# Kernel tuning notes

Measured on AMD Instinct MI355X. Metric: run time of the kernel, lower is better.

## Reference

```python
import jax, jax.numpy as jnp
import numpy as np

D = 1024
H = 16
DK = D // H


def setup_inputs() -> dict:
    key = jax.random.key(0)
    ks = jax.random.split(key, 5)
    B, S = 4, 2048
    scale = 1.0 / np.sqrt(D)
    return {
        "inputs": jax.random.normal(ks[0], (B, S, D), dtype=jnp.float32),
        "mask": jnp.ones((B, S), dtype=jnp.int32),
        "Wq": jax.random.normal(ks[1], (D, D), dtype=jnp.float32) * scale,
        "Wk": jax.random.normal(ks[2], (D, D), dtype=jnp.float32) * scale,
        "Wv": jax.random.normal(ks[3], (D, D), dtype=jnp.float32) * scale,
        "Wo": jax.random.normal(ks[4], (D, D), dtype=jnp.float32) * scale,
    }


def reference(inputs, mask, Wq, Wk, Wv, Wo):
    B, S, _ = inputs.shape

    def split_heads(x):  # [B,S,D] -> [B,H,S,DK]
        return x.reshape(B, S, H, DK).transpose(0, 2, 1, 3)

    q = split_heads(inputs @ Wq)
    k = split_heads(inputs @ Wk)
    v = split_heads(inputs @ Wv)

    scores = jnp.einsum("bhqd,bhkd->bhqk", q, k) / jnp.sqrt(jnp.float32(DK))
    m = mask.astype(jnp.float32)[:, None, None, :]  # [B,1,1,S] over key axis
    scores = scores + (1.0 - m) * -1e9
    attn = jax.nn.softmax(scores, axis=-1)
    out = jnp.einsum("bhqk,bhkd->bhqd", attn, v)
    out = out.transpose(0, 2, 1, 3).reshape(B, S, D)
    return out @ Wo
```

## Files before the change

### kernel.cpp

```cpp
#include <hip/hip_runtime.h>
#include <hip/hip_bf16.h>
#include <stdint.h>

#define S_LEN 2048
#define D_DIM 1024
#define NH    16
#define DKH   64
#define BATCH 4

typedef __bf16 bf16x8 __attribute__((ext_vector_type(8)));
typedef float  f32x4  __attribute__((ext_vector_type(4)));

__device__ __forceinline__ unsigned short f2bf(float x) {
  unsigned u = __float_as_uint(x);
  return (unsigned short)((u + 0x7FFFu + ((u >> 16) & 1u)) >> 16);
}
__device__ __forceinline__ float bf2f(unsigned short b) {
  return __uint_as_float(((unsigned)b) << 16);
}

__device__ __forceinline__ void gll16(const void* g, void* l) {
  __builtin_amdgcn_global_load_lds((const __attribute__((address_space(1))) unsigned*)g,
                                   (__attribute__((address_space(3))) unsigned*)l, 16, 0, 0);
}

#define MFMA(a, b, c) __builtin_amdgcn_mfma_f32_16x16x32_bf16(a, b, c, 0, 0, 0)

__global__ void k_split(const float4* __restrict__ x, ushort4* __restrict__ hi,
                        ushort4* __restrict__ lo, int n4) {
  int i = blockIdx.x * 256 + threadIdx.x;
  if (i >= n4) return;
  float4 v = x[i];
  ushort4 h, l;
  h.x = f2bf(v.x); l.x = f2bf(v.x - bf2f(h.x));
  h.y = f2bf(v.y); l.y = f2bf(v.y - bf2f(h.y));
  h.z = f2bf(v.z); l.z = f2bf(v.z - bf2f(h.z));
  h.w = f2bf(v.w); l.w = f2bf(v.w - bf2f(h.w));
  hi[i] = h;
  lo[i] = l;
}

__global__ void k_wt(const float* __restrict__ W, unsigned short* __restrict__ hi,
                     unsigned short* __restrict__ lo) {
  __shared__ float t[64][65];
  const int tid = threadIdx.x;
  const int k0 = blockIdx.x * 64, n0 = blockIdx.y * 64;
#pragma unroll
  for (int i = 0; i < 16; i++) {
    int idx = i * 256 + tid;
    int r = idx >> 6, c = idx & 63;
    t[r][c] = W[(size_t)(k0 + r) * D_DIM + n0 + c];
  }
  __syncthreads();
#pragma unroll
  for (int i = 0; i < 16; i++) {
    int idx = i * 256 + tid;
    int r = idx >> 6, c = idx & 63;
    float v = t[c][r];
    unsigned short h = f2bf(v);
    size_t o = (size_t)(n0 + r) * D_DIM + k0 + c;
    hi[o] = h;
    lo[o] = f2bf(v - bf2f(h));
  }
}

template <int MODE>
__global__ __launch_bounds__(256, 2) void gemm_hilo(
    const unsigned short* __restrict__ Ahi, const unsigned short* __restrict__ Alo,
    const unsigned short* __restrict__ Bth, const unsigned short* __restrict__ Btl,
    unsigned short* __restrict__ Chi, unsigned short* __restrict__ Clo,
    float* __restrict__ Cf, float escale) {
  constexpr int N = 1024, K = 1024;
  extern __shared__ char smem[];
  char* sAh = smem;
  char* sAl = smem + 16384;
  char* sBh = smem + 32768;
  char* sBl = smem + 49152;

  const int tid = threadIdx.x;
  const int lane = tid & 63, w = tid >> 6;
  const int wr = w >> 1, wc = w & 1;
  const int m0 = blockIdx.y * 128, n0 = blockIdx.x * 128;

  int gofs[4], lofs[4];
#pragma unroll
  for (int i = 0; i < 4; i++) {
    int c = (w * 4 + i) * 64 + lane;
    int row = c >> 3, s = c & 7;
    int sp = s ^ (row & 7);
    gofs[i] = row * K + sp * 8;
    lofs[i] = (w * 4 + i) * 1024;
  }
  const unsigned short* pAh = Ahi + (size_t)m0 * K;
  const unsigned short* pAl = Alo + (size_t)m0 * K;
  const unsigned short* pBh = Bth + (size_t)n0 * K;
  const unsigned short* pBl = Btl + (size_t)n0 * K;

  f32x4 acc[4][4] = {};

  for (int kt = 0; kt < K / 64; ++kt) {
    const int ko = kt * 64;
#pragma unroll
    for (int i = 0; i < 4; i++) {
      gll16(pAh + ko + gofs[i], sAh + lofs[i]);
      gll16(pAl + ko + gofs[i], sAl + lofs[i]);
      gll16(pBh + ko + gofs[i], sBh + lofs[i]);
      gll16(pBl + ko + gofs[i], sBl + lofs[i]);
    }
    __syncthreads();
#pragma unroll
    for (int kk = 0; kk < 2; kk++) {
      bf16x8 ah[4], al[4], bh[4], bl[4];
      const int cch = kk * 4 + (lane >> 4);
#pragma unroll
      for (int mr = 0; mr < 4; mr++) {
        int row = wr * 64 + mr * 16 + (lane & 15);
        int off = row * 128 + ((cch ^ (row & 7)) << 4);
        ah[mr] = *(const bf16x8*)(sAh + off);
        al[mr] = *(const bf16x8*)(sAl + off);
      }
#pragma unroll
      for (int nr = 0; nr < 4; nr++) {
        int row = wc * 64 + nr * 16 + (lane & 15);
        int off = row * 128 + ((cch ^ (row & 7)) << 4);
        bh[nr] = *(const bf16x8*)(sBh + off);
        bl[nr] = *(const bf16x8*)(sBl + off);
      }
#pragma unroll
      for (int mr = 0; mr < 4; mr++)
#pragma unroll
        for (int nr = 0; nr < 4; nr++) {
          acc[mr][nr] = MFMA(ah[mr], bh[nr], acc[mr][nr]);
          acc[mr][nr] = MFMA(ah[mr], bl[nr], acc[mr][nr]);
          acc[mr][nr] = MFMA(al[mr], bh[nr], acc[mr][nr]);
        }
    }
    __syncthreads();
  }

#pragma unroll
  for (int mr = 0; mr < 4; mr++)
#pragma unroll
    for (int nr = 0; nr < 4; nr++)
#pragma unroll
      for (int j = 0; j < 4; j++) {
        int row = m0 + wr * 64 + mr * 16 + (lane >> 4) * 4 + j;
        int col = n0 + wc * 64 + nr * 16 + (lane & 15);
        float v = acc[mr][nr][j];
        if constexpr (MODE == 0) {
          v *= escale;
          size_t o = (size_t)row * N + col;
          unsigned short h = f2bf(v);
          Chi[o] = h;
          Clo[o] = f2bf(v - bf2f(h));
        } else if constexpr (MODE == 1) {
          int bi = row >> 11, s = row & (S_LEN - 1);
          int hh = col >> 6, d = col & (DKH - 1);
          size_t o = ((size_t)(bi * NH + hh) * DKH + d) * S_LEN + s;
          unsigned short h = f2bf(v);
          Chi[o] = h;
          Clo[o] = f2bf(v - bf2f(h));
        } else {
          Cf[(size_t)row * N + col] = v;
        }
      }
}

__global__ __launch_bounds__(256, 2) void attn4(
    const unsigned short* __restrict__ Qh, const unsigned short* __restrict__ Ql,
    const unsigned short* __restrict__ Kh, const unsigned short* __restrict__ Kl,
    const unsigned short* __restrict__ Vth, const unsigned short* __restrict__ Vtl,
    const int* __restrict__ mask,
    unsigned short* __restrict__ Oh, unsigned short* __restrict__ Ol) {
  __shared__ char sKh0[8192], sKl0[8192], sVh0[8192], sVl0[8192];
  __shared__ char sKh1[8192], sKl1[8192], sVh1[8192], sVl1[8192];
  __shared__ char sP[4][4096];

  const int tid = threadIdx.x, lane = tid & 63, w = tid >> 6;
  const int bh = blockIdx.x, b = bh >> 4, h = bh & (NH - 1);
  const int q0 = blockIdx.y * 128 + w * 32;
  const int lo16 = lane & 15, hi4 = lane >> 4;

  bf16x8 qh[2][2], ql[2][2];
#pragma unroll
  for (int g = 0; g < 2; g++)
#pragma unroll
    for (int kk = 0; kk < 2; kk++) {
      size_t base = ((size_t)(b * S_LEN + q0 + g * 16 + lo16)) * D_DIM + h * DKH + kk * 32 + hi4 * 8;
      qh[g][kk] = *(const bf16x8*)(Qh + base);
      ql[g][kk] = *(const bf16x8*)(Ql + base);
    }

  int srowK[2], scolK[2], lofs[2];
#pragma unroll
  for (int i = 0; i < 2; i++) {
    int c = (w * 2 + i) * 64 + lane;
    int row = c >> 3, s = c & 7;
    srowK[i] = row;
    scolK[i] = (s ^ (row & 7)) * 8;
    lofs[i] = c * 16 - lane * 16;
  }

  float lsum[2][4] = {};
  f32x4 oacc[2][4] = {};
  char* sPw = sP[w];

  const size_t kbase = (size_t)b * S_LEN * D_DIM + h * DKH;
  const size_t vbase = (size_t)bh * DKH * S_LEN;
  const int* mrow = mask + b * S_LEN;

  auto STAGE = [&](char* dKh, char* dKl, char* dVh, char* dVl, int sk0) {
#pragma unroll
    for (int i = 0; i < 2; i++) {
      size_t gk = kbase + (size_t)(sk0 + srowK[i]) * D_DIM + scolK[i];
      gll16(Kh + gk, dKh + lofs[i]);
      gll16(Kl + gk, dKl + lofs[i]);
      size_t gv = vbase + (size_t)srowK[i] * S_LEN + sk0 + scolK[i];
      gll16(Vth + gv, dVh + lofs[i]);
      gll16(Vtl + gv, dVl + lofs[i]);
    }
  };

  auto COMPUTE = [&](const char* cKh, const char* cKl, const char* cVh,
                     const char* cVl, int sk0) {
    f32x4 sc[2][4] = {};
    __builtin_amdgcn_s_setprio(1);
#pragma unroll
    for (int nr = 0; nr < 4; nr++) {
      int row = nr * 16 + lo16;
      int off0 = row * 128 + ((hi4 ^ (row & 7)) << 4);
      int off1 = row * 128 + (((4 + hi4) ^ (row & 7)) << 4);
      bf16x8 kh0 = *(const bf16x8*)(cKh + off0);
      bf16x8 kh1 = *(const bf16x8*)(cKh + off1);
      bf16x8 kl0 = *(const bf16x8*)(cKl + off0);
      bf16x8 kl1 = *(const bf16x8*)(cKl + off1);
#pragma unroll
      for (int g = 0; g < 2; g++) {
        sc[g][nr] = MFMA(qh[g][0], kh0, sc[g][nr]);
        sc[g][nr] = MFMA(qh[g][1], kh1, sc[g][nr]);
        sc[g][nr] = MFMA(qh[g][0], kl0, sc[g][nr]);
        sc[g][nr] = MFMA(qh[g][1], kl1, sc[g][nr]);
        sc[g][nr] = MFMA(ql[g][0], kh0, sc[g][nr]);
        sc[g][nr] = MFMA(ql[g][1], kh1, sc[g][nr]);
      }
    }
    __builtin_amdgcn_s_setprio(0);

#pragma unroll
    for (int nr = 0; nr < 4; nr++) {
      float bias = mrow[sk0 + nr * 16 + lo16] ? 0.f : -1e9f;
#pragma unroll
      for (int g = 0; g < 2; g++)
#pragma unroll
        for (int j = 0; j < 4; j++) {
          float p = __expf(sc[g][nr][j] + bias);
          lsum[g][j] += p;
          int row = g * 16 + hi4 * 4 + j;
          int colb = (nr * 16 + lo16) * 2;
          *(unsigned short*)(sPw + row * 128 + (colb ^ ((row & 7) << 4))) = f2bf(p);
        }
    }

    bf16x8 pa[2][2];
#pragma unroll
    for (int g = 0; g < 2; g++)
#pragma unroll
      for (int kk = 0; kk < 2; kk++) {
        int row = g * 16 + lo16;
        int colb = kk * 64 + hi4 * 16;
        pa[g][kk] = *(const bf16x8*)(sPw + row * 128 + (colb ^ ((row & 7) << 4)));
      }

    __builtin_amdgcn_s_setprio(1);
#pragma unroll
    for (int kk = 0; kk < 2; kk++)
#pragma unroll
      for (int f = 0; f < 4; f++) {
        int vrow = f * 16 + lo16;
        int voff = vrow * 128 + (((kk * 4 + hi4) ^ (vrow & 7)) << 4);
        bf16x8 vh = *(const bf16x8*)(cVh + voff);
        bf16x8 vl = *(const bf16x8*)(cVl + voff);
#pragma unroll
        for (int g = 0; g < 2; g++) {
          oacc[g][f] = MFMA(pa[g][kk], vh, oacc[g][f]);
          oacc[g][f] = MFMA(pa[g][kk], vl, oacc[g][f]);
        }
      }
    __builtin_amdgcn_s_setprio(0);
  };

  STAGE(sKh0, sKl0, sVh0, sVl0, 0);
  __syncthreads();

  for (int kt = 0; kt < S_LEN / 64; kt += 2) {
    const int sk0 = kt * 64;
    STAGE(sKh1, sKl1, sVh1, sVl1, sk0 + 64);
    COMPUTE(sKh0, sKl0, sVh0, sVl0, sk0);
    __syncthreads();
    if (kt + 2 < S_LEN / 64) STAGE(sKh0, sKl0, sVh0, sVl0, sk0 + 128);
    COMPUTE(sKh1, sKl1, sVh1, sVl1, sk0 + 64);
    __syncthreads();
  }

  float inv[2][4];
#pragma unroll
  for (int g = 0; g < 2; g++)
#pragma unroll
    for (int j = 0; j < 4; j++) {
      float s = lsum[g][j];
      s += __shfl_xor(s, 1);
      s += __shfl_xor(s, 2);
      s += __shfl_xor(s, 4);
      s += __shfl_xor(s, 8);
      inv[g][j] = 1.f / s;
    }

#pragma unroll
  for (int g = 0; g < 2; g++)
#pragma unroll
    for (int f = 0; f < 4; f++)
#pragma unroll
      for (int j = 0; j < 4; j++) {
        int row = q0 + g * 16 + hi4 * 4 + j;
        int col = h * DKH + f * 16 + lo16;
        float v = oacc[g][f][j] * inv[g][j];
        size_t o = ((size_t)(b * S_LEN + row)) * D_DIM + col;
        unsigned short hh = f2bf(v);
        Oh[o] = hh;
        Ol[o] = f2bf(v - bf2f(hh));
      }
}

extern "C" void kernel_launch(void* const* d_in, const int* in_sizes, int n_in,
                              void* d_out, int out_size, void* d_ws, size_t ws_size,
                              hipStream_t stream) {
  const float* X = (const float*)d_in[0];
  const int* mask = (const int*)d_in[1];
  const float* Wq = (const float*)d_in[2];
  const float* Wk = (const float*)d_in[3];
  const float* Wv = (const float*)d_in[4];
  const float* Wo = (const float*)d_in[5];
  float* out = (float*)d_out;

  const size_t MB = 1024 * 1024;
  if (ws_size < 144 * MB) return;

  char* ws = (char*)d_ws;
  unsigned short* Xh = (unsigned short*)(ws);
  unsigned short* Xl = (unsigned short*)(ws + 16 * MB);
  unsigned short* Wqth = (unsigned short*)(ws + 32 * MB);
  unsigned short* Wqtl = Wqth + 1024 * 1024;
  unsigned short* Wkth = Wqtl + 1024 * 1024;
  unsigned short* Wktl = Wkth + 1024 * 1024;
  unsigned short* Wvth = Wktl + 1024 * 1024;
  unsigned short* Wvtl = Wvth + 1024 * 1024;
  unsigned short* Woth = Wvtl + 1024 * 1024;
  unsigned short* Wotl = Woth + 1024 * 1024;
  unsigned short* Qh = (unsigned short*)(ws + 48 * MB);
  unsigned short* Ql = (unsigned short*)(ws + 64 * MB);
  unsigned short* Kh = (unsigned short*)(ws + 80 * MB);
  unsigned short* Kl = (unsigned short*)(ws + 96 * MB);
  unsigned short* Vth = (unsigned short*)(ws + 112 * MB);
  unsigned short* Vtl = (unsigned short*)(ws + 128 * MB);

  const int n4 = BATCH * S_LEN * D_DIM / 4;
  k_split<<<(n4 + 255) / 256, 256, 0, stream>>>((const float4*)X, (ushort4*)Xh,
                                                (ushort4*)Xl, n4);
  dim3 wtg(16, 16);
  k_wt<<<wtg, 256, 0, stream>>>(Wq, Wqth, Wqtl);
  k_wt<<<wtg, 256, 0, stream>>>(Wk, Wkth, Wktl);
  k_wt<<<wtg, 256, 0, stream>>>(Wv, Wvth, Wvtl);
  k_wt<<<wtg, 256, 0, stream>>>(Wo, Woth, Wotl);

  dim3 gg(8, 64);
  gemm_hilo<0><<<gg, 256, 65536, stream>>>(Xh, Xl, Wqth, Wqtl, Qh, Ql, nullptr, 1.0f);
  gemm_hilo<0><<<gg, 256, 65536, stream>>>(Xh, Xl, Wkth, Wktl, Kh, Kl, nullptr, 0.125f);
  gemm_hilo<1><<<gg, 256, 65536, stream>>>(Xh, Xl, Wvth, Wvtl, Vth, Vtl, nullptr, 1.0f);

  dim3 ag(BATCH * NH, S_LEN / 128);
  attn4<<<ag, 256, 0, stream>>>(Qh, Ql, Kh, Kl, Vth, Vtl, mask, Xh, Xl);

  gemm_hilo<2><<<gg, 256, 65536, stream>>>(Xh, Xl, Woth, Wotl, nullptr, nullptr, out, 1.0f);
}
```

Before: 507.8 us.

## Fuse QKV GEMMs into one launch and shrink attention key tile for occupancy

The three Q/K/V projection GEMMs become a single launch with a 64x24 grid that selects weights and epilogue per block, and the grid is reordered so M varies fastest, which changes L2 reuse of the weight tiles. The attention kernel's key/value tile shrinks from 64 to 32 keys, halving its shared memory so launch bounds can request 4 blocks per SM. The aim is to cut launch gaps and tail waves and to raise attention occupancy. The cost is twice as many barrier and staging iterations in attention.

Measured after the change: 524.5 us. 3.3% more time.

```diff
diff --git a/kernel.cpp b/kernel.cpp
--- a/kernel.cpp
+++ b/kernel.cpp
@@ -64,14 +64,11 @@
   }
 }
 
-template <int MODE>
-__global__ __launch_bounds__(256, 2) void gemm_hilo(
+__device__ __forceinline__ void gemm_core(
     const unsigned short* __restrict__ Ahi, const unsigned short* __restrict__ Alo,
     const unsigned short* __restrict__ Bth, const unsigned short* __restrict__ Btl,
-    unsigned short* __restrict__ Chi, unsigned short* __restrict__ Clo,
-    float* __restrict__ Cf, float escale) {
-  constexpr int N = 1024, K = 1024;
-  extern __shared__ char smem[];
+    int m0, int n0, char* smem, f32x4 (&acc)[4][4]) {
+  constexpr int K = 1024;
   char* sAh = smem;
   char* sAl = smem + 16384;
   char* sBh = smem + 32768;
@@ -80,7 +77,6 @@
   const int tid = threadIdx.x;
   const int lane = tid & 63, w = tid >> 6;
   const int wr = w >> 1, wc = w & 1;
-  const int m0 = blockIdx.y * 128, n0 = blockIdx.x * 128;
 
   int gofs[4], lofs[4];
 #pragma unroll
@@ -96,8 +92,6 @@
   const unsigned short* pBh = Bth + (size_t)n0 * K;
   const unsigned short* pBl = Btl + (size_t)n0 * K;
 
-  f32x4 acc[4][4] = {};
-
   for (int kt = 0; kt < K / 64; ++kt) {
     const int ko = kt * 64;
 #pragma unroll
@@ -137,7 +131,33 @@
     }
     __syncthreads();
   }
-
+}
+
+__global__ __launch_bounds__(256, 2) void gemm_qkv(
+    const unsigned short* __restrict__ Ahi, const unsigned short* __restrict__ Alo,
+    const unsigned short* __restrict__ Wqh, const unsigned short* __restrict__ Wql,
+    const unsigned short* __restrict__ Wkh, const unsigned short* __restrict__ Wkl,
+    const unsigned short* __restrict__ Wvh, const unsigned short* __restrict__ Wvl,
+    unsigned short* __restrict__ Qh, unsigned short* __restrict__ Ql,
+    unsigned short* __restrict__ Kh, unsigned short* __restrict__ Kl,
+    unsigned short* __restrict__ Vth, unsigned short* __restrict__ Vtl) {
+  constexpr int N = 1024;
+  extern __shared__ char smem[];
+  const int m0 = blockIdx.x * 128;
+  const int mat = blockIdx.y >> 3;
+  const int n0 = (blockIdx.y & 7) * 128;
+
+  const unsigned short* Bth = mat == 0 ? Wqh : mat == 1 ? Wkh : Wvh;
+  const unsigned short* Btl = mat == 0 ? Wql : mat == 1 ? Wkl : Wvl;
+  unsigned short* Chi = mat == 0 ? Qh : mat == 1 ? Kh : Vth;
+  unsigned short* Clo = mat == 0 ? Ql : mat == 1 ? Kl : Vtl;
+  const float esc = mat == 1 ? 0.125f : 1.0f;
+
+  f32x4 acc[4][4] = {};
+  gemm_core(Ahi, Alo, Bth, Btl, m0, n0, smem, acc);
+
+  const int lane = threadIdx.x & 63, w = threadIdx.x >> 6;
+  const int wr = w >> 1, wc = w & 1;
 #pragma unroll
   for (int mr = 0; mr < 4; mr++)
 #pragma unroll
@@ -147,34 +167,57 @@
         int row = m0 + wr * 64 + mr * 16 + (lane >> 4) * 4 + j;
         int col = n0 + wc * 64 + nr * 16 + (lane & 15);
         float v = acc[mr][nr][j];
-        if constexpr (MODE == 0) {
-          v *= escale;
+        if (mat < 2) {
+          v *= esc;
           size_t o = (size_t)row * N + col;
-          unsigned short h = f2bf(v);
-          Chi[o] = h;
-          Clo[o] = f2bf(v - bf2f(h));
-        } else if constexpr (MODE == 1) {
+          unsigned short hh = f2bf(v);
+          Chi[o] = hh;
+          Clo[o] = f2bf(v - bf2f(hh));
+        } else {
           int bi = row >> 11, s = row & (S_LEN - 1);
-          int hh = col >> 6, d = col & (DKH - 1);
-          size_t o = ((size_t)(bi * NH + hh) * DKH + d) * S_LEN + s;
-          unsigned short h = f2bf(v);
-          Chi[o] = h;
-          Clo[o] = f2bf(v - bf2f(h));
-        } else {
-          Cf[(size_t)row * N + col] = v;
+          int hh2 = col >> 6, d = col & (DKH - 1);
+          size_t o = ((size_t)(bi * NH + hh2) * DKH + d) * S_LEN + s;
+          unsigned short hh = f2bf(v);
+          Chi[o] = hh;
+          Clo[o] = f2bf(v - bf2f(hh));
         }
       }
 }
 
-__global__ __launch_bounds__(256, 2) void attn4(
+__global__ __launch_bounds__(256, 2) void gemm_wo(
+    const unsigned short* __restrict__ Ahi, const unsigned short* __restrict__ Alo,
+    const unsigned short* __restrict__ Bth, const unsigned short* __restrict__ Btl,
+    float* __restrict__ Cf) {
+  constexpr int N = 1024;
+  extern __shared__ char smem[];
+  const int m0 = blockIdx.x * 128, n0 = blockIdx.y * 128;
+
+  f32x4 acc[4][4] = {};
+  gemm_core(Ahi, Alo, Bth, Btl, m0, n0, smem, acc);
+
+  const int lane = threadIdx.x & 63, w = threadIdx.x >> 6;
+  const int wr = w >> 1, wc = w & 1;
+#pragma unroll
+  for (int mr = 0; mr < 4; mr++)
+#pragma unroll
+    for (int nr = 0; nr < 4; nr++)
+#pragma unroll
+      for (int j = 0; j < 4; j++) {
+        int row = m0 + wr * 64 + mr * 16 + (lane >> 4) * 4 + j;
+        int col = n0 + wc * 64 + nr * 16 + (lane & 15);
+        Cf[(size_t)row * N + col] = acc[mr][nr][j];
+      }
+}
+
+__global__ __launch_bounds__(256, 4) void attn5(
     const unsigned short* __restrict__ Qh, const unsigned short* __restrict__ Ql,
     const unsigned short* __restrict__ Kh, const unsigned short* __restrict__ Kl,
     const unsigned short* __restrict__ Vth, const unsigned short* __restrict__ Vtl,
     const int* __restrict__ mask,
     unsigned short* __restrict__ Oh, unsigned short* __restrict__ Ol) {
-  __shared__ char sKh0[8192], sKl0[8192], sVh0[8192], sVl0[8192];
-  __shared__ char sKh1[8192], sKl1[8192], sVh1[8192], sVl1[8192];
-  __shared__ char sP[4][4096];
+  __shared__ char sKh0[4096], sKl0[4096], sVh0[4096], sVl0[4096];
+  __shared__ char sKh1[4096], sKl1[4096], sVh1[4096], sVl1[4096];
+  __shared__ char sP[4][2048];
 
   const int tid = threadIdx.x, lane = tid & 63, w = tid >> 6;
   const int bh = blockIdx.x, b = bh >> 4, h = bh & (NH - 1);
@@ -191,15 +234,12 @@
       ql[g][kk] = *(const bf16x8*)(Ql + base);
     }
 
-  int srowK[2], scolK[2], lofs[2];
-#pragma unroll
-  for (int i = 0; i < 2; i++) {
-    int c = (w * 2 + i) * 64 + lane;
-    int row = c >> 3, s = c & 7;
-    srowK[i] = row;
-    scolK[i] = (s ^ (row & 7)) * 8;
-    lofs[i] = c * 16 - lane * 16;
-  }
+  const int c = w * 64 + lane;
+  const int krow = c >> 3;
+  const int kcol = ((c & 7) ^ (krow & 7)) * 8;
+  const int vrow = c >> 2;
+  const int vcol = ((c & 3) ^ (vrow & 3)) * 8;
+  const int ldst = w * 1024;
 
   float lsum[2][4] = {};
   f32x4 oacc[2][4] = {};
@@ -210,23 +250,20 @@
   const int* mrow = mask + b * S_LEN;
 
   auto STAGE = [&](char* dKh, char* dKl, char* dVh, char* dVl, int sk0) {
-#pragma unroll
-    for (int i = 0; i < 2; i++) {
-      size_t gk = kbase + (size_t)(sk0 + srowK[i]) * D_DIM + scolK[i];
-      gll16(Kh + gk, dKh + lofs[i]);
-      gll16(Kl + gk, dKl + lofs[i]);
-      size_t gv = vbase + (size_t)srowK[i] * S_LEN + sk0 + scolK[i];
-      gll16(Vth + gv, dVh + lofs[i]);
-      gll16(Vtl + gv, dVl + lofs[i]);
-    }
+    size_t gk = kbase + (size_t)(sk0 + krow) * D_DIM + kcol;
+    gll16(Kh + gk, dKh + ldst);
+    gll16(Kl + gk, dKl + ldst);
+    size_t gv = vbase + (size_t)vrow * S_LEN + sk0 + vcol;
+    gll16(Vth + gv, dVh + ldst);
+    gll16(Vtl + gv, dVl + ldst);
   };
 
   auto COMPUTE = [&](const char* cKh, const char* cKl, const char* cVh,
                      const char* cVl, int sk0) {
-    f32x4 sc[2][4] = {};
+    f32x4 sc[2][2] = {};
     __builtin_amdgcn_s_setprio(1);
 #pragma unroll
-    for (int nr = 0; nr < 4; nr++) {
+    for (int nr = 0; nr < 2; nr++) {
       int row = nr * 16 + lo16;
       int off0 = row * 128 + ((hi4 ^ (row & 7)) << 4);
       int off1 = row * 128 + (((4 + hi4) ^ (row & 7)) << 4);
@@ -247,7 +284,7 @@
     __builtin_amdgcn_s_setprio(0);
 
 #pragma unroll
-    for (int nr = 0; nr < 4; nr++) {
+    for (int nr = 0; nr < 2; nr++) {
       float bias = mrow[sk0 + nr * 16 + lo16] ? 0.f : -1e9f;
 #pragma unroll
       for (int g = 0; g < 2; g++)
@@ -257,48 +294,43 @@
           lsum[g][j] += p;
           int row = g * 16 + hi4 * 4 + j;
           int colb = (nr * 16 + lo16) * 2;
-          *(unsigned short*)(sPw + row * 128 + (colb ^ ((row & 7) << 4))) = f2bf(p);
+          *(unsigned short*)(sPw + row * 64 + (colb ^ ((row & 3) << 4))) = f2bf(p);
         }
     }
 
-    bf16x8 pa[2][2];
-#pragma unroll
-    for (int g = 0; g < 2; g++)
-#pragma unroll
-      for (int kk = 0; kk < 2; kk++) {
-        int row = g * 16 + lo16;
-        int colb = kk * 64 + hi4 * 16;
-        pa[g][kk] = *(const bf16x8*)(sPw + row * 128 + (colb ^ ((row & 7) << 4)));
-      }
+    bf16x8 pa[2];
+#pragma unroll
+    for (int g = 0; g < 2; g++) {
+      int row = g * 16 + lo16;
+      pa[g] = *(const bf16x8*)(sPw + row * 64 + ((hi4 * 16) ^ ((row & 3) << 4)));
+    }
 
     __builtin_amdgcn_s_setprio(1);
 #pragma unroll
-    for (int kk = 0; kk < 2; kk++)
-#pragma unroll
-      for (int f = 0; f < 4; f++) {
-        int vrow = f * 16 + lo16;
-        int voff = vrow * 128 + (((kk * 4 + hi4) ^ (vrow & 7)) << 4);
-        bf16x8 vh = *(const bf16x8*)(cVh + voff);
-        bf16x8 vl = *(const bf16x8*)(cVl + voff);
-#pragma unroll
-        for (int g = 0; g < 2; g++) {
-          oacc[g][f] = MFMA(pa[g][kk], vh, oacc[g][f]);
-          oacc[g][f] = MFMA(pa[g][kk], vl, oacc[g][f]);
-        }
-      }
+    for (int f = 0; f < 4; f++) {
+      int vr = f * 16 + lo16;
+      int voff = vr * 64 + ((hi4 ^ (vr & 3)) << 4);
+      bf16x8 vh = *(const bf16x8*)(cVh + voff);
+      bf16x8 vl = *(const bf16x8*)(cVl + voff);
+#pragma unroll
+      for (int g = 0; g < 2; g++) {
+        oacc[g][f] = MFMA(pa[g], vh, oacc[g][f]);
+        oacc[g][f] = MFMA(pa[g], vl, oacc[g][f]);
+      }
+    }
     __builtin_amdgcn_s_setprio(0);
   };
 
   STAGE(sKh0, sKl0, sVh0, sVl0, 0);
   __syncthreads();
 
-  for (int kt = 0; kt < S_LEN / 64; kt += 2) {
-    const int sk0 = kt * 64;
-    STAGE(sKh1, sKl1, sVh1, sVl1, sk0 + 64);
+  for (int kt = 0; kt < S_LEN / 32; kt += 2) {
+    const int sk0 = kt * 32;
+    STAGE(sKh1, sKl1, sVh1, sVl1, sk0 + 32);
     COMPUTE(sKh0, sKl0, sVh0, sVl0, sk0);
     __syncthreads();
-    if (kt + 2 < S_LEN / 64) STAGE(sKh0, sKl0, sVh0, sVl0, sk0 + 128);
-    COMPUTE(sKh1, sKl1, sVh1, sVl1, sk0 + 64);
+    if (kt + 2 < S_LEN / 32) STAGE(sKh0, sKl0, sVh0, sVl0, sk0 + 64);
+    COMPUTE(sKh1, sKl1, sVh1, sVl1, sk0 + 32);
     __syncthreads();
   }
 
@@ -372,13 +404,11 @@
   k_wt<<<wtg, 256, 0, stream>>>(Wv, Wvth, Wvtl);
   k_wt<<<wtg, 256, 0, stream>>>(Wo, Woth, Wotl);
 
-  dim3 gg(8, 64);
-  gemm_hilo<0><<<gg, 256, 65536, stream>>>(Xh, Xl, Wqth, Wqtl, Qh, Ql, nullptr, 1.0f);
-  gemm_hilo<0><<<gg, 256, 65536, stream>>>(Xh, Xl, Wkth, Wktl, Kh, Kl, nullptr, 0.125f);
-  gemm_hilo<1><<<gg, 256, 65536, stream>>>(Xh, Xl, Wvth, Wvtl, Vth, Vtl, nullptr, 1.0f);
+  gemm_qkv<<<dim3(64, 24), 256, 65536, stream>>>(
+      Xh, Xl, Wqth, Wqtl, Wkth, Wktl, Wvth, Wvtl, Qh, Ql, Kh, Kl, Vth, Vtl);
 
   dim3 ag(BATCH * NH, S_LEN / 128);
-  attn4<<<ag, 256, 0, stream>>>(Qh, Ql, Kh, Kl, Vth, Vtl, mask, Xh, Xl);
-
-  gemm_hilo<2><<<gg, 256, 65536, stream>>>(Xh, Xl, Woth, Wotl, nullptr, nullptr, out, 1.0f);
-}
+  attn5<<<ag, 256, 0, stream>>>(Qh, Ql, Kh, Kl, Vth, Vtl, mask, Xh, Xl);
+
+  gemm_wo<<<dim3(64, 8), 256, 65536, stream>>>(Xh, Xl, Woth, Wotl, out);
+}
```
